# Kernel tuning notes

Measured on AMD Instinct MI355X. Metric: run time of the kernel, lower is better.

## Reference

```python
import jax, jax.numpy as jnp
import numpy as np

EMBED_DIM = 128
WINDOW_SIZE = 128
B, S, D = 2, 2048, EMBED_DIM
NEG_INF = -1e9


def setup_inputs() -> dict:
    key = jax.random.key(0)
    kq, kk, kv = jax.random.split(key, 3)
    q = jax.random.normal(kq, (B, S, D), dtype=jnp.float32)
    k = jax.random.normal(kk, (B, S, D), dtype=jnp.float32)
    v = jax.random.normal(kv, (B, S, D), dtype=jnp.float32)
    return {"q": q, "k": k, "v": v}


def reference(q, k, v):
    # Sliding-window causal attention: token i attends to [i-W, i] inclusive.
    Bq, Sq, Dq = q.shape
    W = WINDOW_SIZE
    scale = Dq ** -0.5
    offsets = jnp.arange(-W, 1)                      # [W+1]
    idx = jnp.arange(Sq)[:, None] + offsets[None, :]  # [S, W+1]
    valid = idx >= 0                                  # mask out-of-range (pre-sequence) keys
    idx_c = jnp.clip(idx, 0, Sq - 1)
    k_win = k[:, idx_c]                               # [B, S, W+1, D]
    v_win = v[:, idx_c]                               # [B, S, W+1, D]
    scores = jnp.einsum('bsd,bswd->bsw', q, k_win) * scale
    scores = jnp.where(valid[None, :, :], scores, NEG_INF)
    attn = jax.nn.softmax(scores, axis=-1)            # [B, S, W+1]
    out = jnp.einsum('bsw,bswd->bsd', attn, v_win)    # [B, S, D]
    return out
```

## Files before the change

kernel.cpp:

```cpp
#include <hip/hip_runtime.h>
#include <math.h>

#define SEQ 2048
#define DIME 128
#define BQ 16
#define NEG_INF -1.0e9f

typedef __attribute__((ext_vector_type(8))) short bf16x8;
typedef __attribute__((ext_vector_type(4))) float f32x4;

static __device__ __forceinline__ short f2b(float x) {
  union { float f; unsigned u; } v; v.f = x;
  unsigned r = v.u + 0x7FFF + ((v.u >> 16) & 1);
  return (short)(r >> 16);
}

template<bool HAS_HI>
static __device__ __forceinline__ void pv_chunk(
    const float (&pLo)[4], const float (&pHi)[4],
    const float* __restrict__ vb, int kget0, int col, int g,
    f32x4 (&o)[8]) {
  bf16x8 pa;
#pragma unroll
  for (int j = 0; j < 8; ++j) {
    const int r = j & 3;
    const int src = (2 * (g & 1) + (j >> 2)) * 16 + col;
    const float plo = __shfl(pLo[r], src);
    float val;
    if (HAS_HI) {
      const float phi = __shfl(pHi[r], src);
      val = (g >= 2) ? phi : plo;
    } else {
      val = (g >= 2) ? 0.0f : plo;
    }
    pa[j] = f2b(val);
  }
#pragma unroll
  for (int dt = 0; dt < 8; ++dt) {
    bf16x8 bv;
#pragma unroll
    for (int j = 0; j < 8; ++j) {
      int kg = kget0 + 8 * g + j;
      kg = kg < 0 ? 0 : (kg > SEQ - 1 ? SEQ - 1 : kg);
      bv[j] = f2b(vb[(size_t)kg * DIME + 16 * dt + col]);
    }
    o[dt] = __builtin_amdgcn_mfma_f32_16x16x32_bf16(pa, bv, o[dt], 0, 0, 0);
  }
}

__global__ __launch_bounds__(256) void swa_mfma_kernel(
    const float* __restrict__ q, const float* __restrict__ k,
    const float* __restrict__ v, float* __restrict__ out) {
  __shared__ float lds_m[4][16];
  __shared__ float lds_s[4][16];
  __shared__ float lds_o[4][16][132];

  const int tid = threadIdx.x;
  const int lane = tid & 63;
  const int w = tid >> 6;
  const int col = lane & 15;
  const int g = lane >> 4;

  const int blk = blockIdx.x;
  const int b = blk >> 7;
  const int qs = (blk & 127) * BQ;
  const int kbase = qs - 128;

  const float* __restrict__ qb = q + (size_t)b * SEQ * DIME;
  const float* __restrict__ kb = k + (size_t)b * SEQ * DIME;
  const float* __restrict__ vb = v + (size_t)b * SEQ * DIME;

  bf16x8 qf[4];
  {
    const float* qrow = qb + (size_t)(qs + col) * DIME + 8 * g;
#pragma unroll
    for (int kc = 0; kc < 4; ++kc) {
      const float4 lo = *(const float4*)(qrow + 32 * kc);
      const float4 hi = *(const float4*)(qrow + 32 * kc + 4);
      bf16x8 f;
      f[0] = f2b(lo.x); f[1] = f2b(lo.y); f[2] = f2b(lo.z); f[3] = f2b(lo.w);
      f[4] = f2b(hi.x); f[5] = f2b(hi.y); f[6] = f2b(hi.z); f[7] = f2b(hi.w);
      qf[kc] = f;
    }
  }

  float sc[3][4];
  const float scale = 0.08838834764831845f;
#pragma unroll
  for (int ti = 0; ti < 3; ++ti) {
    const int t = (ti == 2) ? 8 : 2 * w + ti;
    f32x4 acc = {0.f, 0.f, 0.f, 0.f};
    const int krow = kbase + 16 * t + col;
    const float* krp = kb + (size_t)(krow < 0 ? 0 : krow) * DIME + 8 * g;
#pragma unroll
    for (int kc = 0; kc < 4; ++kc) {
      const float4 lo = *(const float4*)(krp + 32 * kc);
      const float4 hi = *(const float4*)(krp + 32 * kc + 4);
      bf16x8 a;
      a[0] = f2b(lo.x); a[1] = f2b(lo.y); a[2] = f2b(lo.z); a[3] = f2b(lo.w);
      a[4] = f2b(hi.x); a[5] = f2b(hi.y); a[6] = f2b(hi.z); a[7] = f2b(hi.w);
      acc = __builtin_amdgcn_mfma_f32_16x16x32_bf16(a, qf[kc], acc, 0, 0, 0);
    }
#pragma unroll
    for (int r = 0; r < 4; ++r) {
      const int kg = kbase + 16 * t + 4 * g + r;
      const int qg = qs + col;
      const bool valid = (kg >= 0) && (kg >= qg - 128) && (kg <= qg) &&
                         (ti != 2 || w == 0);
      sc[ti][r] = valid ? acc[r] * scale : NEG_INF;
    }
  }

  float m = NEG_INF;
#pragma unroll
  for (int ti = 0; ti < 3; ++ti)
#pragma unroll
    for (int r = 0; r < 4; ++r) m = fmaxf(m, sc[ti][r]);
  m = fmaxf(m, __shfl_xor(m, 16));
  m = fmaxf(m, __shfl_xor(m, 32));
  float s = 0.f;
#pragma unroll
  for (int ti = 0; ti < 3; ++ti)
#pragma unroll
    for (int r = 0; r < 4; ++r) {
      const float p = __expf(sc[ti][r] - m);
      sc[ti][r] = p;
      s += p;
    }
  s += __shfl_xor(s, 16);
  s += __shfl_xor(s, 32);
  if (lane < 16) { lds_m[w][lane] = m; lds_s[w][lane] = s; }

  f32x4 o[8];
#pragma unroll
  for (int dt = 0; dt < 8; ++dt) o[dt] = (f32x4){0.f, 0.f, 0.f, 0.f};
  pv_chunk<true>(sc[0], sc[1], vb, kbase + 32 * w, col, g, o);
  if (w == 0) pv_chunk<false>(sc[2], sc[2], vb, kbase + 128, col, g, o);

  __syncthreads();

#pragma unroll
  for (int r = 0; r < 4; ++r) {
    const int ql = 4 * g + r;
    float M = lds_m[0][ql];
    M = fmaxf(M, lds_m[1][ql]);
    M = fmaxf(M, lds_m[2][ql]);
    M = fmaxf(M, lds_m[3][ql]);
    const float wgt = __expf(lds_m[w][ql] - M);
#pragma unroll
    for (int dt = 0; dt < 8; ++dt)
      lds_o[w][ql][16 * dt + col] = o[dt][r] * wgt;
  }
  __syncthreads();

  {
    const int f = tid * 8;
    const int ql = f >> 7;
    const int d0 = f & 127;
    float M = lds_m[0][ql];
    M = fmaxf(M, lds_m[1][ql]);
    M = fmaxf(M, lds_m[2][ql]);
    M = fmaxf(M, lds_m[3][ql]);
    float St = 0.f;
#pragma unroll
    for (int ww = 0; ww < 4; ++ww)
      St += lds_s[ww][ql] * __expf(lds_m[ww][ql] - M);
    const float inv = 1.0f / St;
    f32x4 acc0 = {0.f, 0.f, 0.f, 0.f}, acc1 = {0.f, 0.f, 0.f, 0.f};
#pragma unroll
    for (int ww = 0; ww < 4; ++ww) {
      acc0 += *(const f32x4*)&lds_o[ww][ql][d0];
      acc1 += *(const f32x4*)&lds_o[ww][ql][d0 + 4];
    }
    acc0 *= inv;
    acc1 *= inv;
    float* op = out + (size_t)(b * SEQ + qs + ql) * DIME + d0;
    *(f32x4*)op = acc0;
    *(f32x4*)(op + 4) = acc1;
  }
}

extern "C" void kernel_launch(void* const* d_in, const int* in_sizes, int n_in,
                              void* d_out, int out_size, void* d_ws, size_t ws_size,
                              hipStream_t stream) {
  const float* q = (const float*)d_in[0];
  const float* k = (const float*)d_in[1];
  const float* v = (const float*)d_in[2];
  float* out = (float*)d_out;
  dim3 grid(256), block(256);
  swa_mfma_kernel<<<grid, block, 0, stream>>>(q, k, v, out);
}
```

Before: 13.48 us.

## Halve query tile, split PV across waves by head-dim slice with LDS P

Reduces queries per block to 8 and doubles the grid to 512 blocks of 512 threads. Each of the 8 waves computes one key tile of scores and writes exp-scores to LDS. A block-wide pass rescales P by the global max, and each wave then computes a 16-column slice of the output over all keys, with V prefetched into registers at kernel start. This removes the cross-wave output reduction through LDS and exposes more parallelism, but half of each 16-row MFMA is wasted on padded query rows and an extra barrier plus LDS traffic for P is added.

New measurement: 19.85 us. +47.3%, slower.

```diff
diff --git a/kernel.cpp b/kernel.cpp
--- a/kernel.cpp
+++ b/kernel.cpp
@@ -3,7 +3,7 @@
 
 #define SEQ 2048
 #define DIME 128
-#define BQ 16
+#define BQ 8
 #define NEG_INF -1.0e9f
 
 typedef __attribute__((ext_vector_type(8))) short bf16x8;
@@ -15,45 +15,13 @@
   return (short)(r >> 16);
 }
 
-template<bool HAS_HI>
-static __device__ __forceinline__ void pv_chunk(
-    const float (&pLo)[4], const float (&pHi)[4],
-    const float* __restrict__ vb, int kget0, int col, int g,
-    f32x4 (&o)[8]) {
-  bf16x8 pa;
-#pragma unroll
-  for (int j = 0; j < 8; ++j) {
-    const int r = j & 3;
-    const int src = (2 * (g & 1) + (j >> 2)) * 16 + col;
-    const float plo = __shfl(pLo[r], src);
-    float val;
-    if (HAS_HI) {
-      const float phi = __shfl(pHi[r], src);
-      val = (g >= 2) ? phi : plo;
-    } else {
-      val = (g >= 2) ? 0.0f : plo;
-    }
-    pa[j] = f2b(val);
-  }
-#pragma unroll
-  for (int dt = 0; dt < 8; ++dt) {
-    bf16x8 bv;
-#pragma unroll
-    for (int j = 0; j < 8; ++j) {
-      int kg = kget0 + 8 * g + j;
-      kg = kg < 0 ? 0 : (kg > SEQ - 1 ? SEQ - 1 : kg);
-      bv[j] = f2b(vb[(size_t)kg * DIME + 16 * dt + col]);
-    }
-    o[dt] = __builtin_amdgcn_mfma_f32_16x16x32_bf16(pa, bv, o[dt], 0, 0, 0);
-  }
-}
-
-__global__ __launch_bounds__(256) void swa_mfma_kernel(
+__global__ __launch_bounds__(512, 4) void swa_kernel(
     const float* __restrict__ q, const float* __restrict__ k,
     const float* __restrict__ v, float* __restrict__ out) {
-  __shared__ float lds_m[4][16];
-  __shared__ float lds_s[4][16];
-  __shared__ float lds_o[4][16][132];
+  __shared__ float P[160][17];
+  __shared__ float mW[9][16];
+  __shared__ float sW[9][16];
+  __shared__ __attribute__((aligned(16))) float Sinv[16];
 
   const int tid = threadIdx.x;
   const int lane = tid & 63;
@@ -62,21 +30,32 @@
   const int g = lane >> 4;
 
   const int blk = blockIdx.x;
-  const int b = blk >> 7;
-  const int qs = (blk & 127) * BQ;
+  const int b = blk >> 8;
+  const int qs = (blk & 255) * BQ;
   const int kbase = qs - 128;
 
   const float* __restrict__ qb = q + (size_t)b * SEQ * DIME;
   const float* __restrict__ kb = k + (size_t)b * SEQ * DIME;
   const float* __restrict__ vb = v + (size_t)b * SEQ * DIME;
 
+  float bvf[5][8];
+#pragma unroll
+  for (int c = 0; c < 5; ++c)
+#pragma unroll
+    for (int j = 0; j < 8; ++j) {
+      int kg = kbase + 32 * c + 8 * g + j;
+      kg = kg < 0 ? 0 : (kg > SEQ - 1 ? SEQ - 1 : kg);
+      bvf[c][j] = vb[(size_t)kg * DIME + 16 * w + col];
+    }
+
   bf16x8 qf[4];
   {
-    const float* qrow = qb + (size_t)(qs + col) * DIME + 8 * g;
+    int qr = qs + col; qr = qr > SEQ - 1 ? SEQ - 1 : qr;
+    const float* qrow = qb + (size_t)qr * DIME + 8 * g;
 #pragma unroll
     for (int kc = 0; kc < 4; ++kc) {
-      const float4 lo = *(const float4*)(qrow + 32 * kc);
-      const float4 hi = *(const float4*)(qrow + 32 * kc + 4);
+      float4 lo = *(const float4*)(qrow + 32 * kc);
+      float4 hi = *(const float4*)(qrow + 32 * kc + 4);
       bf16x8 f;
       f[0] = f2b(lo.x); f[1] = f2b(lo.y); f[2] = f2b(lo.z); f[3] = f2b(lo.w);
       f[4] = f2b(hi.x); f[5] = f2b(hi.y); f[6] = f2b(hi.z); f[7] = f2b(hi.w);
@@ -84,99 +63,87 @@
     }
   }
 
-  float sc[3][4];
   const float scale = 0.08838834764831845f;
-#pragma unroll
-  for (int ti = 0; ti < 3; ++ti) {
-    const int t = (ti == 2) ? 8 : 2 * w + ti;
+  const int ntile = (w == 7) ? 2 : 1;
+  for (int ti = 0; ti < ntile; ++ti) {
+    const int t = (ti == 0) ? w : 8;
     f32x4 acc = {0.f, 0.f, 0.f, 0.f};
-    const int krow = kbase + 16 * t + col;
-    const float* krp = kb + (size_t)(krow < 0 ? 0 : krow) * DIME + 8 * g;
+    int krow = kbase + 16 * t + col;
+    krow = krow < 0 ? 0 : (krow > SEQ - 1 ? SEQ - 1 : krow);
+    const float* krp = kb + (size_t)krow * DIME + 8 * g;
 #pragma unroll
     for (int kc = 0; kc < 4; ++kc) {
-      const float4 lo = *(const float4*)(krp + 32 * kc);
-      const float4 hi = *(const float4*)(krp + 32 * kc + 4);
+      float4 lo = *(const float4*)(krp + 32 * kc);
+      float4 hi = *(const float4*)(krp + 32 * kc + 4);
       bf16x8 a;
       a[0] = f2b(lo.x); a[1] = f2b(lo.y); a[2] = f2b(lo.z); a[3] = f2b(lo.w);
       a[4] = f2b(hi.x); a[5] = f2b(hi.y); a[6] = f2b(hi.z); a[7] = f2b(hi.w);
       acc = __builtin_amdgcn_mfma_f32_16x16x32_bf16(a, qf[kc], acc, 0, 0, 0);
     }
+    float sc[4];
+    float m = NEG_INF;
 #pragma unroll
     for (int r = 0; r < 4; ++r) {
       const int kg = kbase + 16 * t + 4 * g + r;
       const int qg = qs + col;
-      const bool valid = (kg >= 0) && (kg >= qg - 128) && (kg <= qg) &&
-                         (ti != 2 || w == 0);
-      sc[ti][r] = valid ? acc[r] * scale : NEG_INF;
+      const bool valid = (col < BQ) && (kg >= 0) && (kg >= qg - 128) && (kg <= qg);
+      sc[r] = valid ? acc[r] * scale : NEG_INF;
+      m = fmaxf(m, sc[r]);
+    }
+    m = fmaxf(m, __shfl_xor(m, 16));
+    m = fmaxf(m, __shfl_xor(m, 32));
+    float s = 0.f;
+#pragma unroll
+    for (int r = 0; r < 4; ++r) { sc[r] = __expf(sc[r] - m); s += sc[r]; }
+    s += __shfl_xor(s, 16);
+    s += __shfl_xor(s, 32);
+    if (g == 0) { mW[t][col] = m; sW[t][col] = s; }
+#pragma unroll
+    for (int r = 0; r < 4; ++r) P[16 * t + 4 * g + r][col] = sc[r];
+  }
+
+  __syncthreads();
+
+  {
+    const int qq = tid & 15;
+    const int ks = tid >> 4;
+    float M = mW[0][qq];
+#pragma unroll
+    for (int t = 1; t < 9; ++t) M = fmaxf(M, mW[t][qq]);
+    if (ks == 0) {
+      float St = 0.f;
+#pragma unroll
+      for (int t = 0; t < 9; ++t) St += sW[t][qq] * __expf(mW[t][qq] - M);
+      Sinv[qq] = 1.0f / St;
+    }
+#pragma unroll
+    for (int i = 0; i < 5; ++i) {
+      const int key = ks + 32 * i;
+      if (key < 144) P[key][qq] *= __expf(mW[key >> 4][qq] - M);
+      else           P[key][qq] = 0.f;
     }
   }
 
-  float m = NEG_INF;
-#pragma unroll
-  for (int ti = 0; ti < 3; ++ti)
-#pragma unroll
-    for (int r = 0; r < 4; ++r) m = fmaxf(m, sc[ti][r]);
-  m = fmaxf(m, __shfl_xor(m, 16));
-  m = fmaxf(m, __shfl_xor(m, 32));
-  float s = 0.f;
-#pragma unroll
-  for (int ti = 0; ti < 3; ++ti)
-#pragma unroll
-    for (int r = 0; r < 4; ++r) {
-      const float p = __expf(sc[ti][r] - m);
-      sc[ti][r] = p;
-      s += p;
-    }
-  s += __shfl_xor(s, 16);
-  s += __shfl_xor(s, 32);
-  if (lane < 16) { lds_m[w][lane] = m; lds_s[w][lane] = s; }
-
-  f32x4 o[8];
-#pragma unroll
-  for (int dt = 0; dt < 8; ++dt) o[dt] = (f32x4){0.f, 0.f, 0.f, 0.f};
-  pv_chunk<true>(sc[0], sc[1], vb, kbase + 32 * w, col, g, o);
-  if (w == 0) pv_chunk<false>(sc[2], sc[2], vb, kbase + 128, col, g, o);
-
   __syncthreads();
 
+  f32x4 o = {0.f, 0.f, 0.f, 0.f};
+#pragma unroll
+  for (int c = 0; c < 5; ++c) {
+    bf16x8 pa, bv;
+#pragma unroll
+    for (int j = 0; j < 8; ++j) {
+      pa[j] = f2b(P[32 * c + 8 * g + j][col]);
+      bv[j] = f2b(bvf[c][j]);
+    }
+    o = __builtin_amdgcn_mfma_f32_16x16x32_bf16(pa, bv, o, 0, 0, 0);
+  }
+
+  const f32x4 sv = *(const f32x4*)&Sinv[4 * g];
 #pragma unroll
   for (int r = 0; r < 4; ++r) {
-    const int ql = 4 * g + r;
-    float M = lds_m[0][ql];
-    M = fmaxf(M, lds_m[1][ql]);
-    M = fmaxf(M, lds_m[2][ql]);
-    M = fmaxf(M, lds_m[3][ql]);
-    const float wgt = __expf(lds_m[w][ql] - M);
-#pragma unroll
-    for (int dt = 0; dt < 8; ++dt)
-      lds_o[w][ql][16 * dt + col] = o[dt][r] * wgt;
-  }
-  __syncthreads();
-
-  {
-    const int f = tid * 8;
-    const int ql = f >> 7;
-    const int d0 = f & 127;
-    float M = lds_m[0][ql];
-    M = fmaxf(M, lds_m[1][ql]);
-    M = fmaxf(M, lds_m[2][ql]);
-    M = fmaxf(M, lds_m[3][ql]);
-    float St = 0.f;
-#pragma unroll
-    for (int ww = 0; ww < 4; ++ww)
-      St += lds_s[ww][ql] * __expf(lds_m[ww][ql] - M);
-    const float inv = 1.0f / St;
-    f32x4 acc0 = {0.f, 0.f, 0.f, 0.f}, acc1 = {0.f, 0.f, 0.f, 0.f};
-#pragma unroll
-    for (int ww = 0; ww < 4; ++ww) {
-      acc0 += *(const f32x4*)&lds_o[ww][ql][d0];
-      acc1 += *(const f32x4*)&lds_o[ww][ql][d0 + 4];
-    }
-    acc0 *= inv;
-    acc1 *= inv;
-    float* op = out + (size_t)(b * SEQ + qs + ql) * DIME + d0;
-    *(f32x4*)op = acc0;
-    *(f32x4*)(op + 4) = acc1;
+    const int qrow = 4 * g + r;
+    if (qrow < BQ)
+      out[(size_t)(b * SEQ + qs + qrow) * DIME + 16 * w + col] = o[r] * sv[r];
   }
 }
 
@@ -187,6 +154,6 @@
   const float* k = (const float*)d_in[1];
   const float* v = (const float*)d_in[2];
   float* out = (float*)d_out;
-  dim3 grid(256), block(256);
-  swa_mfma_kernel<<<grid, block, 0, stream>>>(q, k, v, out);
+  dim3 grid(512), block(512);
+  swa_kernel<<<grid, block, 0, stream>>>(q, k, v, out);
 }
```
